# Optimization experiments

Measured on AMD Instinct MI355X. Metric: run time of the kernel, lower is better.

The kernel has to match this reference:

```python
import jax, jax.numpy as jnp
import numpy as np

ENC_DIM, DEC_DIM, ATT_DIM = 2048, 512, 512
B, L = 64, 1024


def setup_inputs() -> dict:
    key = jax.random.key(0)
    ks = jax.random.split(key, 8)
    s_enc = 1.0 / np.sqrt(ENC_DIM)
    s_dec = 1.0 / np.sqrt(DEC_DIM)
    s_att = 1.0 / np.sqrt(ATT_DIM)
    return {
        "encoder_out": jax.random.normal(ks[0], (B, L, ENC_DIM), jnp.float32),
        "decoder_hidden": jax.random.normal(ks[1], (B, DEC_DIM), jnp.float32),
        "W_enc": jax.random.uniform(ks[2], (ENC_DIM, ATT_DIM), jnp.float32, -s_enc, s_enc),
        "b_enc": jax.random.uniform(ks[3], (ATT_DIM,), jnp.float32, -s_enc, s_enc),
        "W_dec": jax.random.uniform(ks[4], (DEC_DIM, ATT_DIM), jnp.float32, -s_dec, s_dec),
        "b_dec": jax.random.uniform(ks[5], (ATT_DIM,), jnp.float32, -s_dec, s_dec),
        "W_full": jax.random.uniform(ks[6], (ATT_DIM,), jnp.float32, -s_att, s_att),
        "b_full": jax.random.uniform(ks[7], (), jnp.float32, -s_att, s_att),
    }


def reference(encoder_out, decoder_hidden, W_enc, b_enc, W_dec, b_dec, W_full, b_full):
    # att1: [B, L, A]
    att1 = jnp.einsum('ble,ea->bla', encoder_out, W_enc) + b_enc
    # att2: [B, A]
    att2 = decoder_hidden @ W_dec + b_dec
    # scores: [B, L]
    att = jnp.einsum('bla,a->bl', jnp.tanh(att1 + att2[:, None, :]), W_full) + b_full
    alpha = jax.nn.softmax(att, axis=1)
    # NOTE: faithful to source -- weighted sum is over att1, not encoder_out.
    attention_weighted_encoding = jnp.einsum('bla,bl->ba', att1, alpha)
    return attention_weighted_encoding, alpha
```

## Files before the change

kernel.cpp:

```cpp
#include <hip/hip_runtime.h>
#include <hip/hip_bf16.h>


#define Bn 64
#define Ln 1024
#define En 2048
#define An 512
#define TM 64
#define NTILES (Ln/TM)
#define AWE_OFF 0
#define ALPHA_OFF (Bn*An)
#define TILEB 8192

using short8 = __attribute__((ext_vector_type(8))) short;
using sh4    = __attribute__((ext_vector_type(4))) short;
using f32x4  = __attribute__((ext_vector_type(4))) float;

__device__ inline short f2bf(float x){
    unsigned u = __builtin_bit_cast(unsigned, x);
    unsigned r = (u + 0x7fffu + ((u >> 16) & 1u)) >> 16;
    return (short)r;
}
__device__ inline float tanh_fast(float x){
    return 2.0f * __frcp_rn(1.0f + __expf(-2.0f * x)) - 1.0f;
}

__global__ __launch_bounds__(256) void k_prep(const float* __restrict__ W,
                                              unsigned short* __restrict__ Wp,
                                              const float* __restrict__ dh,
                                              const float* __restrict__ Wd,
                                              const float* __restrict__ bd,
                                              float* __restrict__ att2){
    __shared__ float dl[512];
    int blk = blockIdx.x, tid = threadIdx.x;
    if (blk < 512){
        int t = blk * 256 + tid;
        int f = t >> 6, lane = t & 63;
        int kb = f >> 5, nc = f & 31;
        int k0 = kb * 32 + (lane >> 4) * 8;
        int col = nc * 16 + (lane & 15);
        short8 v;
#pragma unroll
        for (int j = 0; j < 8; ++j)
            v[j] = f2bf(W[(size_t)(k0 + j) * An + col]);
        *(short8*)(Wp + (size_t)f * 512 + lane * 8) = v;
    } else {
        int b = blk - 512;
        dl[tid]       = dh[b * 512 + tid];
        dl[tid + 256] = dh[b * 512 + tid + 256];
        __syncthreads();
        for (int a = tid; a < An; a += 256){
            float s = bd[a];
            for (int k = 0; k < 512; ++k)
                s = fmaf(dl[k], Wd[(size_t)k * An + a], s);
            att2[b * An + a] = s;
        }
    }
}


#define MFMA(a, b, c) __builtin_amdgcn_mfma_f32_16x16x32_bf16((a), (b), (c), 0, 0, 0)

#define BLOAD(S, P)                                                           \
    { int pc = (P) > 31 ? 31 : (P);                                           \
      const unsigned short* bp = Bbase + (size_t)pc * 32768;                  \
      S##00 = *(const short8*)(bp);                                           \
      S##01 = *(const short8*)(bp + 512);                                     \
      S##10 = *(const short8*)(bp + 16384);                                   \
      S##11 = *(const short8*)(bp + 16384 + 512); }

#define STAGE(Q, R)                                                           \
    { sh4 sv;                                                                 \
      sv[0] = f2bf(R.x); sv[1] = f2bf(R.y);                                   \
      sv[2] = f2bf(R.z); sv[3] = f2bf(R.w);                                   \
      *(sh4*)(swp + (Q) * TILEB) = sv; }

#define MFMAS(Q, S)                                                           \
    _Pragma("unroll")                                                         \
    for (int mi = 0; mi < 4; ++mi){                                           \
        short8 af0 = *(const short8*)(as0 + (Q) * TILEB + mi * 2048);         \
        short8 af1 = *(const short8*)(as1 + (Q) * TILEB + mi * 2048);         \
        acc[mi][0] = MFMA(af0, S##00, acc[mi][0]);                            \
        acc[mi][1] = MFMA(af0, S##01, acc[mi][1]);                            \
        acc[mi][0] = MFMA(af1, S##10, acc[mi][0]);                            \
        acc[mi][1] = MFMA(af1, S##11, acc[mi][1]);                            \
    }

__global__ __launch_bounds__(1024)
void k_main(const float* __restrict__ enc, const unsigned short* __restrict__ Wp,
            const float* __restrict__ benc, const float* __restrict__ att2,
            const float* __restrict__ wfull, float* __restrict__ out,
            float* __restrict__ pawe_ws, float* __restrict__ ms_ws){
    const int wg   = blockIdx.x;
    const int b    = wg >> 4;
    const int tile = wg & 15;
    const int l0   = tile * TM;
    const int tid  = threadIdx.x;
    const int lane = tid & 63, w = tid >> 6;

    __shared__ alignas(16) unsigned short Alds[4][TM * 64];
    __shared__ float red[16][TM];
    __shared__ float plds[TM];
    char* const alds = (char*)Alds;

    f32x4 acc[4][2];
#pragma unroll
    for (int mi = 0; mi < 4; ++mi)
#pragma unroll
        for (int ni = 0; ni < 2; ++ni)
            acc[mi][ni] = (f32x4){0.f, 0.f, 0.f, 0.f};

    const int srow  = tid >> 4;
    const int sbyte = srow * 128 + (((tid & 15) * 8) ^ ((srow & 7) << 4));
    char* const swp = alds + sbyte;
    const float* apt = enc + ((size_t)(b * Ln + l0 + srow)) * En + (tid & 15) * 4;

    const unsigned short* Bbase = Wp + (size_t)(w * 2) * 512 + lane * 8;

    const int arow = lane & 15;
    const int akb  = (lane >> 4) * 16;
    const int sw   = (arow & 7) << 4;
    const char* const as0 = alds + arow * 128 + (akb ^ sw);
    const char* const as1 = alds + arow * 128 + ((64 + akb) ^ sw);

    short8 fa00, fa01, fa10, fa11;
    short8 fb00, fb01, fb10, fb11;

    float4 ra = *(const float4*)(apt);
    float4 rb = *(const float4*)(apt + 64);
    STAGE(0, ra)
    STAGE(1, rb)
    ra = *(const float4*)(apt + 2 * 64);
    rb = *(const float4*)(apt + 3 * 64);
    BLOAD(fa, 0)

    for (int p = 0; p < 32; p += 4){
        __syncthreads();
        {
            BLOAD(fb, p + 1)
            STAGE(2, ra)
            STAGE(3, rb)
            int t0 = p + 4 > 31 ? 31 : p + 4;
            int t1 = p + 5 > 31 ? 31 : p + 5;
            ra = *(const float4*)(apt + t0 * 64);
            rb = *(const float4*)(apt + t1 * 64);
            MFMAS(0, fa)
        }
        {
            BLOAD(fa, p + 2)
            MFMAS(1, fb)
        }
        __syncthreads();
        {
            BLOAD(fb, p + 3)
            STAGE(0, ra)
            STAGE(1, rb)
            int t0 = p + 6 > 31 ? 31 : p + 6;
            int t1 = p + 7 > 31 ? 31 : p + 7;
            ra = *(const float4*)(apt + t0 * 64);
            rb = *(const float4*)(apt + t1 * 64);
            MFMAS(2, fa)
        }
        {
            BLOAD(fa, p + 4)
            MFMAS(3, fb)
        }
    }

    float be[2], a2[2], wfv[2];
    const int cbase = w * 32 + (lane & 15);
#pragma unroll
    for (int ni = 0; ni < 2; ++ni){
        int c = cbase + ni * 16;
        be[ni]  = benc[c];
        a2[ni]  = att2[b * An + c];
        wfv[ni] = wfull[c];
    }

    float tsum[4][4];
#pragma unroll
    for (int mi = 0; mi < 4; ++mi)
#pragma unroll
        for (int j = 0; j < 4; ++j)
            tsum[mi][j] = 0.f;
#pragma unroll
    for (int mi = 0; mi < 4; ++mi)
#pragma unroll
        for (int ni = 0; ni < 2; ++ni)
#pragma unroll
            for (int j = 0; j < 4; ++j){
                float vv = acc[mi][ni][j] + be[ni];
                acc[mi][ni][j] = vv;
                tsum[mi][j] += tanh_fast(vv + a2[ni]) * wfv[ni];
            }

#pragma unroll
    for (int mi = 0; mi < 4; ++mi)
#pragma unroll
        for (int j = 0; j < 4; ++j){
            float t = tsum[mi][j];
            t += __shfl_xor(t, 1); t += __shfl_xor(t, 2);
            t += __shfl_xor(t, 4); t += __shfl_xor(t, 8);
            if ((lane & 15) == 0)
                red[w][mi * 16 + (lane >> 4) * 4 + j] = t;
        }
    __syncthreads();

    if (tid < 64){
        float s = 0.f;
#pragma unroll
        for (int k = 0; k < 16; ++k)
            s += red[k][tid];
        out[ALPHA_OFF + b * Ln + l0 + tid] = s;
        float m = s;
        m = fmaxf(m, __shfl_xor(m, 1));  m = fmaxf(m, __shfl_xor(m, 2));
        m = fmaxf(m, __shfl_xor(m, 4));  m = fmaxf(m, __shfl_xor(m, 8));
        m = fmaxf(m, __shfl_xor(m, 16)); m = fmaxf(m, __shfl_xor(m, 32));
        float pv = __expf(s - m);
        float sm = pv;
        sm += __shfl_xor(sm, 1);  sm += __shfl_xor(sm, 2);
        sm += __shfl_xor(sm, 4);  sm += __shfl_xor(sm, 8);
        sm += __shfl_xor(sm, 16); sm += __shfl_xor(sm, 32);
        plds[tid] = pv;
        if (tid == 0){ ms_ws[wg * 2] = m; ms_ws[wg * 2 + 1] = sm; }
    }
    __syncthreads();

    float pp0 = 0.f, pp1 = 0.f;
#pragma unroll
    for (int mi = 0; mi < 4; ++mi)
#pragma unroll
        for (int j = 0; j < 4; ++j){
            float pr = plds[mi * 16 + (lane >> 4) * 4 + j];
            pp0 += pr * acc[mi][0][j];
            pp1 += pr * acc[mi][1][j];
        }
    pp0 += __shfl_xor(pp0, 16); pp0 += __shfl_xor(pp0, 32);
    pp1 += __shfl_xor(pp1, 16); pp1 += __shfl_xor(pp1, 32);
    if (lane < 16){
        pawe_ws[(size_t)wg * An + w * 32 + lane]      = pp0;
        pawe_ws[(size_t)wg * An + w * 32 + 16 + lane] = pp1;
    }
}

__global__ __launch_bounds__(256) void k_final(const float* __restrict__ pawe,
                                               const float* __restrict__ ms,
                                               float* __restrict__ out){
    int b = blockIdx.x, tid = threadIdx.x;
    __shared__ float scale[NTILES];
    __shared__ float sh[2];
    if (tid < 64){
        int lane = tid;
        float m = -1e30f, su = 0.f;
        if (lane < NTILES){ m = ms[(b * NTILES + lane) * 2]; su = ms[(b * NTILES + lane) * 2 + 1]; }
        float mm = m;
        mm = fmaxf(mm, __shfl_xor(mm, 1)); mm = fmaxf(mm, __shfl_xor(mm, 2));
        mm = fmaxf(mm, __shfl_xor(mm, 4)); mm = fmaxf(mm, __shfl_xor(mm, 8));
        float sc = (lane < NTILES) ? su * __expf(m - mm) : 0.f;
        float tot = sc;
        tot += __shfl_xor(tot, 1); tot += __shfl_xor(tot, 2);
        tot += __shfl_xor(tot, 4); tot += __shfl_xor(tot, 8);
        if (lane < NTILES) scale[lane] = __expf(m - mm);
        if (lane == 0){ sh[0] = 1.0f / tot; sh[1] = mm; }
    }
    __syncthreads();
    float inv = sh[0], mm = sh[1];
    for (int a = tid; a < An; a += 256){
        float s = 0.f;
#pragma unroll
        for (int t = 0; t < NTILES; ++t)
            s += pawe[((size_t)(b * NTILES + t)) * An + a] * scale[t];
        out[AWE_OFF + b * An + a] = s * inv;
    }
    for (int l = tid; l < Ln; l += 256){
        float s = out[ALPHA_OFF + b * Ln + l];
        out[ALPHA_OFF + b * Ln + l] = __expf(s - mm) * inv;
    }
}

extern "C" void kernel_launch(void* const* d_in, const int* in_sizes, int n_in,
                              void* d_out, int out_size, void* d_ws, size_t ws_size,
                              hipStream_t stream){
    const float* enc   = (const float*)d_in[0];
    const float* dh    = (const float*)d_in[1];
    const float* Wenc  = (const float*)d_in[2];
    const float* benc  = (const float*)d_in[3];
    const float* Wdec  = (const float*)d_in[4];
    const float* bdec  = (const float*)d_in[5];
    const float* wfull = (const float*)d_in[6];
    float* out = (float*)d_out;

    char* ws = (char*)d_ws;
    unsigned short* Wp = (unsigned short*)ws;
    float* att2 = (float*)(ws + (2u << 20));
    float* pawe = (float*)(ws + (2u << 20) + (128u << 10));
    float* msb  = (float*)(ws + (4u << 20) + (128u << 10));

    k_prep<<<576, 256, 0, stream>>>(Wenc, Wp, dh, Wdec, bdec, att2);
    k_main<<<Bn * NTILES, 1024, 0, stream>>>(enc, Wp, benc, att2, wfull, out, pawe, msb);
    k_final<<<Bn, 256, 0, stream>>>(pawe, msb, out);
}
```

Measured before the change: 246.8 us.

## Halve k_main block size and give each wave 64 output columns

The main GEMM kernel now launches 512 threads (8 waves) instead of 1024. Each wave computes 4 N-fragments (64 columns) instead of 2, which doubles register accumulators and B-fragment loads per wave and reuses each A fragment read from LDS across more MFMAs. The staging path also widens to 8 floats per thread, written to LDS as one short8 store. The aim is fewer LDS reads per MFMA and less per-wave overhead, at the cost of higher register pressure and fewer waves to hide memory latency.

```diff
diff --git a/kernel.cpp b/kernel.cpp
--- a/kernel.cpp
+++ b/kernel.cpp
@@ -13,7 +13,6 @@
 #define TILEB 8192
 
 using short8 = __attribute__((ext_vector_type(8))) short;
-using sh4    = __attribute__((ext_vector_type(4))) short;
 using f32x4  = __attribute__((ext_vector_type(4))) float;
 
 __device__ inline short f2bf(float x){
@@ -66,14 +65,20 @@
       const unsigned short* bp = Bbase + (size_t)pc * 32768;                  \
       S##00 = *(const short8*)(bp);                                           \
       S##01 = *(const short8*)(bp + 512);                                     \
+      S##02 = *(const short8*)(bp + 1024);                                    \
+      S##03 = *(const short8*)(bp + 1536);                                    \
       S##10 = *(const short8*)(bp + 16384);                                   \
-      S##11 = *(const short8*)(bp + 16384 + 512); }
-
-#define STAGE(Q, R)                                                           \
-    { sh4 sv;                                                                 \
-      sv[0] = f2bf(R.x); sv[1] = f2bf(R.y);                                   \
-      sv[2] = f2bf(R.z); sv[3] = f2bf(R.w);                                   \
-      *(sh4*)(swp + (Q) * TILEB) = sv; }
+      S##11 = *(const short8*)(bp + 16384 + 512);                             \
+      S##12 = *(const short8*)(bp + 16384 + 1024);                            \
+      S##13 = *(const short8*)(bp + 16384 + 1536); }
+
+#define STAGE(Q, R0, R1)                                                      \
+    { short8 sv;                                                              \
+      sv[0] = f2bf(R0.x); sv[1] = f2bf(R0.y);                                 \
+      sv[2] = f2bf(R0.z); sv[3] = f2bf(R0.w);                                 \
+      sv[4] = f2bf(R1.x); sv[5] = f2bf(R1.y);                                 \
+      sv[6] = f2bf(R1.z); sv[7] = f2bf(R1.w);                                 \
+      *(short8*)(swp + (Q) * TILEB) = sv; }
 
 #define MFMAS(Q, S)                                                           \
     _Pragma("unroll")                                                         \
@@ -82,11 +87,15 @@
         short8 af1 = *(const short8*)(as1 + (Q) * TILEB + mi * 2048);         \
         acc[mi][0] = MFMA(af0, S##00, acc[mi][0]);                            \
         acc[mi][1] = MFMA(af0, S##01, acc[mi][1]);                            \
+        acc[mi][2] = MFMA(af0, S##02, acc[mi][2]);                            \
+        acc[mi][3] = MFMA(af0, S##03, acc[mi][3]);                            \
         acc[mi][0] = MFMA(af1, S##10, acc[mi][0]);                            \
         acc[mi][1] = MFMA(af1, S##11, acc[mi][1]);                            \
-    }
-
-__global__ __launch_bounds__(1024)
+        acc[mi][2] = MFMA(af1, S##12, acc[mi][2]);                            \
+        acc[mi][3] = MFMA(af1, S##13, acc[mi][3]);                            \
+    }
+
+__global__ __launch_bounds__(512)
 void k_main(const float* __restrict__ enc, const unsigned short* __restrict__ Wp,
             const float* __restrict__ benc, const float* __restrict__ att2,
             const float* __restrict__ wfull, float* __restrict__ out,
@@ -99,23 +108,23 @@
     const int lane = tid & 63, w = tid >> 6;
 
     __shared__ alignas(16) unsigned short Alds[4][TM * 64];
-    __shared__ float red[16][TM];
+    __shared__ float red[8][TM];
     __shared__ float plds[TM];
     char* const alds = (char*)Alds;
 
-    f32x4 acc[4][2];
-#pragma unroll
-    for (int mi = 0; mi < 4; ++mi)
-#pragma unroll
-        for (int ni = 0; ni < 2; ++ni)
+    f32x4 acc[4][4];
+#pragma unroll
+    for (int mi = 0; mi < 4; ++mi)
+#pragma unroll
+        for (int ni = 0; ni < 4; ++ni)
             acc[mi][ni] = (f32x4){0.f, 0.f, 0.f, 0.f};
 
-    const int srow  = tid >> 4;
-    const int sbyte = srow * 128 + (((tid & 15) * 8) ^ ((srow & 7) << 4));
+    const int srow  = tid >> 3;
+    const int sbyte = srow * 128 + (((tid & 7) * 16) ^ ((srow & 7) << 4));
     char* const swp = alds + sbyte;
-    const float* apt = enc + ((size_t)(b * Ln + l0 + srow)) * En + (tid & 15) * 4;
-
-    const unsigned short* Bbase = Wp + (size_t)(w * 2) * 512 + lane * 8;
+    const float* apt = enc + ((size_t)(b * Ln + l0 + srow)) * En + (tid & 7) * 8;
+
+    const unsigned short* Bbase = Wp + (size_t)(w * 4) * 512 + lane * 8;
 
     const int arow = lane & 15;
     const int akb  = (lane >> 4) * 16;
@@ -123,27 +132,33 @@
     const char* const as0 = alds + arow * 128 + (akb ^ sw);
     const char* const as1 = alds + arow * 128 + ((64 + akb) ^ sw);
 
-    short8 fa00, fa01, fa10, fa11;
-    short8 fb00, fb01, fb10, fb11;
-
-    float4 ra = *(const float4*)(apt);
-    float4 rb = *(const float4*)(apt + 64);
-    STAGE(0, ra)
-    STAGE(1, rb)
-    ra = *(const float4*)(apt + 2 * 64);
-    rb = *(const float4*)(apt + 3 * 64);
+    short8 fa00, fa01, fa02, fa03, fa10, fa11, fa12, fa13;
+    short8 fb00, fb01, fb02, fb03, fb10, fb11, fb12, fb13;
+
+    float4 ra0 = *(const float4*)(apt);
+    float4 ra1 = *(const float4*)(apt + 4);
+    float4 rb0 = *(const float4*)(apt + 64);
+    float4 rb1 = *(const float4*)(apt + 68);
+    STAGE(0, ra0, ra1)
+    STAGE(1, rb0, rb1)
+    ra0 = *(const float4*)(apt + 2 * 64);
+    ra1 = *(const float4*)(apt + 2 * 64 + 4);
+    rb0 = *(const float4*)(apt + 3 * 64);
+    rb1 = *(const float4*)(apt + 3 * 64 + 4);
     BLOAD(fa, 0)
 
     for (int p = 0; p < 32; p += 4){
         __syncthreads();
         {
             BLOAD(fb, p + 1)
-            STAGE(2, ra)
-            STAGE(3, rb)
+            STAGE(2, ra0, ra1)
+            STAGE(3, rb0, rb1)
             int t0 = p + 4 > 31 ? 31 : p + 4;
             int t1 = p + 5 > 31 ? 31 : p + 5;
-            ra = *(const float4*)(apt + t0 * 64);
-            rb = *(const float4*)(apt + t1 * 64);
+            ra0 = *(const float4*)(apt + t0 * 64);
+            ra1 = *(const float4*)(apt + t0 * 64 + 4);
+            rb0 = *(const float4*)(apt + t1 * 64);
+            rb1 = *(const float4*)(apt + t1 * 64 + 4);
             MFMAS(0, fa)
         }
         {
@@ -153,12 +168,14 @@
         __syncthreads();
         {
             BLOAD(fb, p + 3)
-            STAGE(0, ra)
-            STAGE(1, rb)
+            STAGE(0, ra0, ra1)
+            STAGE(1, rb0, rb1)
             int t0 = p + 6 > 31 ? 31 : p + 6;
             int t1 = p + 7 > 31 ? 31 : p + 7;
-            ra = *(const float4*)(apt + t0 * 64);
-            rb = *(const float4*)(apt + t1 * 64);
+            ra0 = *(const float4*)(apt + t0 * 64);
+            ra1 = *(const float4*)(apt + t0 * 64 + 4);
+            rb0 = *(const float4*)(apt + t1 * 64);
+            rb1 = *(const float4*)(apt + t1 * 64 + 4);
             MFMAS(2, fa)
         }
         {
@@ -167,10 +184,10 @@
         }
     }
 
-    float be[2], a2[2], wfv[2];
-    const int cbase = w * 32 + (lane & 15);
-#pragma unroll
-    for (int ni = 0; ni < 2; ++ni){
+    float be[4], a2[4], wfv[4];
+    const int cbase = w * 64 + (lane & 15);
+#pragma unroll
+    for (int ni = 0; ni < 4; ++ni){
         int c = cbase + ni * 16;
         be[ni]  = benc[c];
         a2[ni]  = att2[b * An + c];
@@ -186,7 +203,7 @@
 #pragma unroll
     for (int mi = 0; mi < 4; ++mi)
 #pragma unroll
-        for (int ni = 0; ni < 2; ++ni)
+        for (int ni = 0; ni < 4; ++ni)
 #pragma unroll
             for (int j = 0; j < 4; ++j){
                 float vv = acc[mi][ni][j] + be[ni];
@@ -209,7 +226,7 @@
     if (tid < 64){
         float s = 0.f;
 #pragma unroll
-        for (int k = 0; k < 16; ++k)
+        for (int k = 0; k < 8; ++k)
             s += red[k][tid];
         out[ALPHA_OFF + b * Ln + l0 + tid] = s;
         float m = s;
@@ -226,20 +243,27 @@
     }
     __syncthreads();
 
-    float pp0 = 0.f, pp1 = 0.f;
+    float pp[4];
+#pragma unroll
+    for (int ni = 0; ni < 4; ++ni) pp[ni] = 0.f;
 #pragma unroll
     for (int mi = 0; mi < 4; ++mi)
 #pragma unroll
         for (int j = 0; j < 4; ++j){
             float pr = plds[mi * 16 + (lane >> 4) * 4 + j];
-            pp0 += pr * acc[mi][0][j];
-            pp1 += pr * acc[mi][1][j];
-        }
-    pp0 += __shfl_xor(pp0, 16); pp0 += __shfl_xor(pp0, 32);
-    pp1 += __shfl_xor(pp1, 16); pp1 += __shfl_xor(pp1, 32);
+#pragma unroll
+            for (int ni = 0; ni < 4; ++ni)
+                pp[ni] += pr * acc[mi][ni][j];
+        }
+#pragma unroll
+    for (int ni = 0; ni < 4; ++ni){
+        pp[ni] += __shfl_xor(pp[ni], 16);
+        pp[ni] += __shfl_xor(pp[ni], 32);
+    }
     if (lane < 16){
-        pawe_ws[(size_t)wg * An + w * 32 + lane]      = pp0;
-        pawe_ws[(size_t)wg * An + w * 32 + 16 + lane] = pp1;
+#pragma unroll
+        for (int ni = 0; ni < 4; ++ni)
+            pawe_ws[(size_t)wg * An + w * 64 + ni * 16 + lane] = pp[ni];
     }
 }
 
@@ -297,6 +321,6 @@
     float* msb  = (float*)(ws + (4u << 20) + (128u << 10));
 
     k_prep<<<576, 256, 0, stream>>>(Wenc, Wp, dh, Wdec, bdec, att2);
-    k_main<<<Bn * NTILES, 1024, 0, stream>>>(enc, Wp, benc, att2, wfull, out, pawe, msb);
+    k_main<<<Bn * NTILES, 512, 0, stream>>>(enc, Wp, benc, att2, wfull, out, pawe, msb);
     k_final<<<Bn, 256, 0, stream>>>(pawe, msb, out);
 }
```

After: 333.4 us. 35.1% more time.

## Restructure main GEMM loop into double-buffered phases with raw barriers and setprio

Applied to the files above, without the earlier changes.

Replaces the four-slot LDS staging ring with a two-slot ping-pong and unrolls the K loop into uniform phases. Each phase issues the next weight fragment loads, stages the next activation slice to LDS, and prefetches activations four phases ahead in registers. It then runs the MFMAs at raised wave priority and ends with a hand-written lgkmcnt wait plus s_barrier. The aim is to hide global and LDS latency better, halve the LDS footprint, and cut barrier cost. In exchange there is one barrier per phase instead of one per two, and more registers are held for the prefetch.

```diff
diff --git a/kernel.cpp b/kernel.cpp
--- a/kernel.cpp
+++ b/kernel.cpp
@@ -62,8 +62,7 @@
 #define MFMA(a, b, c) __builtin_amdgcn_mfma_f32_16x16x32_bf16((a), (b), (c), 0, 0, 0)
 
 #define BLOAD(S, P)                                                           \
-    { int pc = (P) > 31 ? 31 : (P);                                           \
-      const unsigned short* bp = Bbase + (size_t)pc * 32768;                  \
+    { const unsigned short* bp = Bbase + (size_t)(P) * 32768;                 \
       S##00 = *(const short8*)(bp);                                           \
       S##01 = *(const short8*)(bp + 512);                                     \
       S##10 = *(const short8*)(bp + 16384);                                   \
@@ -85,6 +84,19 @@
         acc[mi][0] = MFMA(af1, S##10, acc[mi][0]);                            \
         acc[mi][1] = MFMA(af1, S##11, acc[mi][1]);                            \
     }
+
+#define PBAR asm volatile("s_waitcnt lgkmcnt(0)\n\ts_barrier" ::: "memory")
+
+#define PHASE(P, QC, QN, SLOT, FC, FN)                                        \
+{                                                                             \
+    BLOAD(FN, ((P) + 1 > 31 ? 31 : (P) + 1))                                  \
+    STAGE(QN, SLOT)                                                           \
+    SLOT = *(const float4*)(apt + ((P) + 5 > 31 ? 31 : (P) + 5) * 64);        \
+    __builtin_amdgcn_s_setprio(1);                                            \
+    MFMAS(QC, FC)                                                             \
+    __builtin_amdgcn_s_setprio(0);                                            \
+    PBAR;                                                                     \
+}
 
 __global__ __launch_bounds__(1024)
 void k_main(const float* __restrict__ enc, const unsigned short* __restrict__ Wp,
@@ -98,7 +110,7 @@
     const int tid  = threadIdx.x;
     const int lane = tid & 63, w = tid >> 6;
 
-    __shared__ alignas(16) unsigned short Alds[4][TM * 64];
+    __shared__ alignas(16) unsigned short Alds[2][TM * 64];
     __shared__ float red[16][TM];
     __shared__ float plds[TM];
     char* const alds = (char*)Alds;
@@ -126,45 +138,23 @@
     short8 fa00, fa01, fa10, fa11;
     short8 fb00, fb01, fb10, fb11;
 
-    float4 ra = *(const float4*)(apt);
-    float4 rb = *(const float4*)(apt + 64);
-    STAGE(0, ra)
-    STAGE(1, rb)
-    ra = *(const float4*)(apt + 2 * 64);
-    rb = *(const float4*)(apt + 3 * 64);
+    float4 S0, S1, S2, S3;
+
+    float4 e0 = *(const float4*)(apt);
+    S1 = *(const float4*)(apt + 64);
+    S2 = *(const float4*)(apt + 128);
+    S3 = *(const float4*)(apt + 192);
+    S0 = *(const float4*)(apt + 256);
     BLOAD(fa, 0)
-
-    for (int p = 0; p < 32; p += 4){
-        __syncthreads();
-        {
-            BLOAD(fb, p + 1)
-            STAGE(2, ra)
-            STAGE(3, rb)
-            int t0 = p + 4 > 31 ? 31 : p + 4;
-            int t1 = p + 5 > 31 ? 31 : p + 5;
-            ra = *(const float4*)(apt + t0 * 64);
-            rb = *(const float4*)(apt + t1 * 64);
-            MFMAS(0, fa)
-        }
-        {
-            BLOAD(fa, p + 2)
-            MFMAS(1, fb)
-        }
-        __syncthreads();
-        {
-            BLOAD(fb, p + 3)
-            STAGE(0, ra)
-            STAGE(1, rb)
-            int t0 = p + 6 > 31 ? 31 : p + 6;
-            int t1 = p + 7 > 31 ? 31 : p + 7;
-            ra = *(const float4*)(apt + t0 * 64);
-            rb = *(const float4*)(apt + t1 * 64);
-            MFMAS(2, fa)
-        }
-        {
-            BLOAD(fa, p + 4)
-            MFMAS(3, fb)
-        }
+    STAGE(0, e0)
+    PBAR;
+
+    for (int sp = 0; sp < 8; ++sp){
+        const int p = sp * 4;
+        PHASE(p + 0, 0, 1, S1, fa, fb)
+        PHASE(p + 1, 1, 0, S2, fb, fa)
+        PHASE(p + 2, 0, 1, S3, fa, fb)
+        PHASE(p + 3, 1, 0, S0, fb, fa)
     }
 
     float be[2], a2[2], wfv[2];
```

Result: no change. 247.8 us, median of 2 (+0.4%).
